# Optimization experiments

Measured on AMD Instinct MI355X. Metric: run time of the kernel, lower is better.

## Reference

```python
import jax, jax.numpy as jnp
import numpy as np

N_HEAD = 16
MASK_VALUE = -10000.0


def setup_inputs() -> dict:
    key = jax.random.key(0)
    k1, k2, k3 = jax.random.split(key, 3)
    B, S, D = 2, 2048, 1024
    x = jax.random.normal(k1, (B, S, D), dtype=jnp.float32)
    W_qkv = jax.random.normal(k2, (D, 3 * D), dtype=jnp.float32) * 0.02
    b_qkv = jnp.zeros((3 * D,), dtype=jnp.float32)
    W_out = jax.random.normal(k3, (D, D), dtype=jnp.float32) * 0.02
    b_out = jnp.zeros((D,), dtype=jnp.float32)
    return {"x": x, "W_qkv": W_qkv, "b_qkv": b_qkv, "W_out": W_out, "b_out": b_out}


def reference(x, W_qkv, b_qkv, W_out, b_out):
    B, S, D = x.shape
    H = N_HEAD
    hd = D // H
    # fused QKV projection
    qkv = x @ W_qkv + b_qkv                      # [B, S, 3D]
    q, k, v = jnp.split(qkv, 3, axis=-1)
    # split heads -> [B, H, S, hd]
    def split_heads(t):
        return t.reshape(B, S, H, hd).transpose(0, 2, 1, 3)
    q, k, v = split_heads(q), split_heads(k), split_heads(v)
    # scaled causal attention with explicit mask-fill (matches ops.attention)
    scale = 1.0 / jnp.sqrt(jnp.asarray(hd, dtype=x.dtype))
    w = jnp.einsum('bhqd,bhkd->bhqk', q, k) * scale   # [B, H, S, S]
    causal = jnp.tril(jnp.ones((S, S), dtype=bool))    # [S, S]
    w = jnp.where(causal, w, jnp.asarray(MASK_VALUE, dtype=w.dtype))
    a = jax.nn.softmax(w, axis=-1)
    o = jnp.einsum('bhqk,bhkd->bhqd', a, v)            # [B, H, S, hd]
    # merge heads -> [B, S, D]
    o = o.transpose(0, 2, 1, 3).reshape(B, S, D)
    out = o @ W_out + b_out
    return out
```

## Files before the change

kernel.cpp:

```cpp
#include <hip/hip_runtime.h>
#include <hip/hip_bf16.h>
#include <stdint.h>

#define BATCH 2
#define SEQ   2048
#define DIM   1024
#define NH    16
#define HD    64
#define MVAL  (-10000.0f)

typedef __attribute__((ext_vector_type(8))) short bf16x8;
typedef __attribute__((ext_vector_type(4))) float f32x4;
typedef unsigned short u16;

static __device__ __forceinline__ u16 f2bf(float f) {
  union { float f; uint32_t u; } c; c.f = f;
  uint32_t x = c.u;
  return (u16)((x + 0x7fffu + ((x >> 16) & 1u)) >> 16);
}

static __device__ __forceinline__ uint32_t pk2(float a, float b) {
  __hip_bfloat162 h = __float22bfloat162_rn(make_float2(a, b));
  union { __hip_bfloat162 h; uint32_t u; } c; c.h = h;
  return c.u;
}

static __device__ __forceinline__ int swz128(int row, int chunk) {
  return row * 128 + (((chunk ^ (row & 7)) & 7) << 4);
}

static __device__ __forceinline__ void gload_lds16(const void* g, void* l) {
  __builtin_amdgcn_global_load_lds((const __attribute__((address_space(1))) void*)g,
                                   (__attribute__((address_space(3))) void*)l, 16, 0, 0);
}

__global__ void cvt_kernel(const float* __restrict__ in, u16* __restrict__ out, int n4) {
  int i = blockIdx.x * blockDim.x + threadIdx.x;
  if (i < n4) {
    float4 v = reinterpret_cast<const float4*>(in)[i];
    reinterpret_cast<uint2*>(out)[i] = make_uint2(pk2(v.x, v.y), pk2(v.z, v.w));
  }
}

__global__ void transpose_cvt_kernel(const float* __restrict__ in, u16* __restrict__ out,
                                     int R, int C) {
  __shared__ float tile[32][33];
  int c0 = blockIdx.x * 32, r0 = blockIdx.y * 32;
  int tx = threadIdx.x, ty = threadIdx.y;
#pragma unroll
  for (int i = 0; i < 32; i += 8)
    tile[ty + i][tx] = in[(size_t)(r0 + ty + i) * C + c0 + tx];
  __syncthreads();
#pragma unroll
  for (int i = 0; i < 32; i += 8)
    out[(size_t)(c0 + ty + i) * R + r0 + tx] = f2bf(tile[tx][ty + i]);
}

template <int EPI>
__global__ __launch_bounds__(256, 2) void gemm_bt_kernel(
    const u16* __restrict__ A, const u16* __restrict__ Bt,
    const float* __restrict__ bias, float* __restrict__ Cout,
    u16* __restrict__ Qo, u16* __restrict__ Ko, u16* __restrict__ Vto,
    int M, int N, int K) {
  __shared__ __align__(16) char lds[32768];
  char* As = lds;
  char* Bs = lds + 16384;
  int tid = threadIdx.x;
  int lane = tid & 63, l15 = lane & 15, l4 = lane >> 4;
  int w = tid >> 6, wr = w >> 1, wc = w & 1;
  int m0 = blockIdx.y * 128, n0 = blockIdx.x * 128;
  int srow = tid >> 3, sch = tid & 7;

  const u16* Ap = A + (size_t)(m0 + srow) * K + sch * 8;
  const u16* Bp = Bt + (size_t)(n0 + srow) * K + sch * 8;

  f32x4 acc[4][4] = {};

  for (int k0 = 0; k0 < K; k0 += 64) {
    __syncthreads();
#pragma unroll
    for (int i = 0; i < 4; i++) {
      gload_lds16(Ap + (size_t)i * 32 * K + k0, As + i * 4096 + tid * 16);
      gload_lds16(Bp + (size_t)i * 32 * K + k0, Bs + i * 4096 + tid * 16);
    }
    __syncthreads();
#pragma unroll
    for (int ks = 0; ks < 2; ks++) {
      int ch = ks * 4 + l4;
      bf16x8 af[4], bfv[4];
#pragma unroll
      for (int mi = 0; mi < 4; mi++)
        af[mi] = *reinterpret_cast<const bf16x8*>(As + (wr * 64 + mi * 16 + l15) * 128 + ch * 16);
#pragma unroll
      for (int nj = 0; nj < 4; nj++)
        bfv[nj] = *reinterpret_cast<const bf16x8*>(Bs + (wc * 64 + nj * 16 + l15) * 128 + ch * 16);
#pragma unroll
      for (int mi = 0; mi < 4; mi++)
#pragma unroll
        for (int nj = 0; nj < 4; nj++)
          acc[mi][nj] = __builtin_amdgcn_mfma_f32_16x16x32_bf16(af[mi], bfv[nj], acc[mi][nj], 0, 0, 0);
    }
  }

#pragma unroll
  for (int nj = 0; nj < 4; nj++) {
    int n = n0 + wc * 64 + nj * 16 + l15;
    float bv = bias[n];
#pragma unroll
    for (int mi = 0; mi < 4; mi++) {
#pragma unroll
      for (int r = 0; r < 4; r++) {
        int m = m0 + wr * 64 + mi * 16 + l4 * 4 + r;
        float v = acc[mi][nj][r] + bv;
        if (EPI == 1) {
          Cout[(size_t)m * N + n] = v;
        } else {
          int b = m >> 11, s = m & 2047;
          int sec = n >> 10, c = n & 1023, h = c >> 6, d = c & 63;
          size_t bh = (size_t)(b * NH + h);
          if (sec == 0)      Qo[(bh * SEQ + s) * HD + d] = f2bf(v * 0.125f);
          else if (sec == 1) Ko[(bh * SEQ + s) * HD + d] = f2bf(v);
          else               Vto[(bh * HD + d) * SEQ + s] = f2bf(v);
        }
      }
    }
  }
}

__global__ __launch_bounds__(256, 2) void attn_kernel(
    const u16* __restrict__ Q, const u16* __restrict__ K,
    const u16* __restrict__ Vt, u16* __restrict__ O) {
  __shared__ __align__(16) char lds[81920];
  int tid = threadIdx.x, lane = tid & 63, w = tid >> 6;
  int l15 = lane & 15, l4 = lane >> 4;
  int sub = w & 1, par = w >> 1;
  int blk = blockIdx.x;
  int bh = (blk & 7) * 4 + ((blk >> 3) & 3);
  int p = blk >> 5;
  const u16* Qh = Q + (size_t)bh * SEQ * HD;
  const u16* Kh = K + (size_t)bh * SEQ * HD;
  const u16* Vh = Vt + (size_t)bh * HD * SEQ;
  char* Pw = lds + 65536 + w * 4096;
  int srow = tid >> 3, sch = tid & 7;
  int b_ = bh >> 4, h_ = bh & 15;

  auto stageKV = [&](int b, int T) {
    const u16* Kt = Kh + (size_t)T * 128 * HD;
    const u16* Vs = Vh + (size_t)T * 128;
    char* Kb = lds + b * 16384;
    char* Vb = lds + 32768 + b * 16384;
#pragma unroll
    for (int i = 0; i < 4; i++) {
      int row = i * 32 + srow;
      int c = (sch ^ (row & 7)) << 3;
      gload_lds16(Kt + (size_t)row * HD + c, Kb + row * 128 + sch * 16);
    }
#pragma unroll
    for (int sv = 0; sv < 2; sv++)
#pragma unroll
      for (int i = 0; i < 2; i++) {
        int d = i * 32 + srow;
        int c = (sch ^ (d & 7)) << 3;
        gload_lds16(Vs + (size_t)d * SEQ + sv * 64 + c, Vb + sv * 8192 + d * 128 + sch * 16);
      }
  };

  int buf = 0;
  stageKV(0, 0);
  __syncthreads();

  for (int pass = 0; pass < 2; pass++) {
    int qt = (pass == 0) ? (31 - p) : p;
    int nT = (qt + 2) >> 1;
    int qb = qt * 64 + sub * 32;

    bf16x8 qf[2][2];
#pragma unroll
    for (int mi = 0; mi < 2; mi++)
#pragma unroll
      for (int ks = 0; ks < 2; ks++)
        qf[mi][ks] = *reinterpret_cast<const bf16x8*>(
            Qh + (size_t)(qb + mi * 16 + l15) * HD + ks * 32 + l4 * 8);

    float mrun[2] = {-1e30f, -1e30f}, lrun[2] = {0.0f, 0.0f};
    f32x4 oacc[4][2] = {};

    for (int T = 0; T < nT; T++) {
      int nxt = (T + 1 < nT) ? (T + 1) : (pass == 0 ? 0 : -1);
      if (nxt >= 0) stageKV(buf ^ 1, nxt);

      char* Kw = lds + buf * 16384 + par * 8192;
      char* Vw = lds + 32768 + buf * 16384 + par * 8192;
      int kvb = T * 128 + par * 64;

      f32x4 s[4][2] = {};
      __builtin_amdgcn_s_setprio(1);
#pragma unroll
      for (int ks = 0; ks < 2; ks++)
#pragma unroll
        for (int nj = 0; nj < 4; nj++) {
          bf16x8 kf = *reinterpret_cast<const bf16x8*>(Kw + swz128(nj * 16 + l15, ks * 4 + l4));
#pragma unroll
          for (int mi = 0; mi < 2; mi++)
            s[nj][mi] = __builtin_amdgcn_mfma_f32_16x16x32_bf16(kf, qf[mi][ks], s[nj][mi], 0, 0, 0);
        }
      __builtin_amdgcn_s_setprio(0);

      if (kvb + 63 > qb) {
#pragma unroll
        for (int nj = 0; nj < 4; nj++)
#pragma unroll
          for (int mi = 0; mi < 2; mi++) {
            int qg = qb + mi * 16 + l15;
#pragma unroll
            for (int r = 0; r < 4; r++) {
              int kg = kvb + nj * 16 + l4 * 4 + r;
              if (kg > qg) s[nj][mi][r] = MVAL;
            }
          }
      }

      float alpha[2];
#pragma unroll
      for (int mi = 0; mi < 2; mi++) {
        float mt = s[0][mi][0];
#pragma unroll
        for (int nj = 0; nj < 4; nj++)
#pragma unroll
          for (int r = 0; r < 4; r++) mt = fmaxf(mt, s[nj][mi][r]);
        mt = fmaxf(mt, __shfl_xor(mt, 16));
        mt = fmaxf(mt, __shfl_xor(mt, 32));
        float mnew = fmaxf(mrun[mi], mt);
        alpha[mi] = __expf(mrun[mi] - mnew);
        mrun[mi] = mnew;
        float rs = 0.0f;
        int prow = mi * 16 + l15;
#pragma unroll
        for (int nj = 0; nj < 4; nj++) {
          float p0 = __expf(s[nj][mi][0] - mnew);
          float p1 = __expf(s[nj][mi][1] - mnew);
          float p2 = __expf(s[nj][mi][2] - mnew);
          float p3 = __expf(s[nj][mi][3] - mnew);
          rs += (p0 + p1) + (p2 + p3);
          int chunk = nj * 2 + (l4 >> 1);
          char* dst = Pw + prow * 128 + (((chunk ^ (prow & 7)) & 7) << 4) + (l4 & 1) * 8;
          *reinterpret_cast<uint2*>(dst) = make_uint2(pk2(p0, p1), pk2(p2, p3));
        }
        rs += __shfl_xor(rs, 16);
        rs += __shfl_xor(rs, 32);
        lrun[mi] = lrun[mi] * alpha[mi] + rs;
      }
#pragma unroll
      for (int nd = 0; nd < 4; nd++)
#pragma unroll
        for (int mi = 0; mi < 2; mi++)
#pragma unroll
          for (int r = 0; r < 4; r++) oacc[nd][mi][r] *= alpha[mi];

      asm volatile("s_waitcnt lgkmcnt(0)" ::: "memory");
      __builtin_amdgcn_sched_barrier(0);

      bf16x8 pf[2][2];
#pragma unroll
      for (int mi = 0; mi < 2; mi++)
#pragma unroll
        for (int ks = 0; ks < 2; ks++)
          pf[mi][ks] = *reinterpret_cast<const bf16x8*>(Pw + swz128(mi * 16 + l15, ks * 4 + l4));

      __builtin_amdgcn_s_setprio(1);
#pragma unroll
      for (int ks = 0; ks < 2; ks++)
#pragma unroll
        for (int nd = 0; nd < 4; nd++) {
          bf16x8 vf = *reinterpret_cast<const bf16x8*>(Vw + swz128(nd * 16 + l15, ks * 4 + l4));
#pragma unroll
          for (int mi = 0; mi < 2; mi++)
            oacc[nd][mi] = __builtin_amdgcn_mfma_f32_16x16x32_bf16(vf, pf[mi][ks], oacc[nd][mi], 0, 0, 0);
        }
      __builtin_amdgcn_s_setprio(0);

      __syncthreads();
      buf ^= 1;
    }

    char* Xo = lds + (buf ^ 1) * 16384;
    float* Xml = (float*)(lds + 65536);
    if (par == 1) {
#pragma unroll
      for (int mi = 0; mi < 2; mi++) {
        int row = sub * 32 + mi * 16 + l15;
        if (l4 == 0) {
          Xml[row * 2] = mrun[mi];
          Xml[row * 2 + 1] = lrun[mi];
        }
#pragma unroll
        for (int nd = 0; nd < 4; nd++)
          *reinterpret_cast<f32x4*>(Xo + row * 256 + (((nd * 4 + l4) ^ (row & 7)) << 4)) =
              oacc[nd][mi];
      }
    }
    __syncthreads();
    if (par == 0) {
#pragma unroll
      for (int mi = 0; mi < 2; mi++) {
        int row = sub * 32 + mi * 16 + l15;
        float mB = Xml[row * 2], lB = Xml[row * 2 + 1];
        float m = fmaxf(mrun[mi], mB);
        float wA = __expf(mrun[mi] - m), wB = __expf(mB - m);
        float linv = 1.0f / (lrun[mi] * wA + lB * wB);
        u16* orow = O + ((size_t)b_ * SEQ + qt * 64 + sub * 32 + mi * 16 + l15) * DIM + h_ * HD;
#pragma unroll
        for (int nd = 0; nd < 4; nd++) {
          f32x4 ob = *reinterpret_cast<const f32x4*>(
              Xo + row * 256 + (((nd * 4 + l4) ^ (row & 7)) << 4));
          float o0 = (oacc[nd][mi][0] * wA + ob[0] * wB) * linv;
          float o1 = (oacc[nd][mi][1] * wA + ob[1] * wB) * linv;
          float o2 = (oacc[nd][mi][2] * wA + ob[2] * wB) * linv;
          float o3 = (oacc[nd][mi][3] * wA + ob[3] * wB) * linv;
          *reinterpret_cast<uint2*>(orow + nd * 16 + l4 * 4) = make_uint2(pk2(o0, o1), pk2(o2, o3));
        }
      }
    }
    __syncthreads();
  }
}

extern "C" void kernel_launch(void* const* d_in, const int* in_sizes, int n_in,
                              void* d_out, int out_size, void* d_ws, size_t ws_size,
                              hipStream_t stream) {
  const float* x     = (const float*)d_in[0];
  const float* W_qkv = (const float*)d_in[1];
  const float* b_qkv = (const float*)d_in[2];
  const float* W_out = (const float*)d_in[3];
  const float* b_out = (const float*)d_in[4];
  float* out = (float*)d_out;
  char* ws = (char*)d_ws;

  u16* xb    = (u16*)(ws);
  u16* WqkvT = (u16*)(ws + 8388608);
  u16* WoutT = (u16*)(ws + 8388608 + 6291456);
  u16* Qb    = (u16*)(ws + 16777216);
  u16* Kb    = (u16*)(ws + 16777216 + 8388608);
  u16* Vtb   = (u16*)(ws + 16777216 + 2 * 8388608);
  u16* Ob    = (u16*)(ws + 16777216 + 3 * 8388608);

  cvt_kernel<<<4096, 256, 0, stream>>>(x, xb, BATCH * SEQ * DIM / 4);
  transpose_cvt_kernel<<<dim3(3 * DIM / 32, DIM / 32), dim3(32, 8), 0, stream>>>(
      W_qkv, WqkvT, DIM, 3 * DIM);
  transpose_cvt_kernel<<<dim3(DIM / 32, DIM / 32), dim3(32, 8), 0, stream>>>(
      W_out, WoutT, DIM, DIM);
  gemm_bt_kernel<0><<<dim3(3 * DIM / 128, BATCH * SEQ / 128), 256, 0, stream>>>(
      xb, WqkvT, b_qkv, nullptr, Qb, Kb, Vtb, BATCH * SEQ, 3 * DIM, DIM);
  attn_kernel<<<512, 256, 0, stream>>>(Qb, Kb, Vtb, Ob);
  gemm_bt_kernel<1><<<dim3(DIM / 128, BATCH * SEQ / 128), 256, 0, stream>>>(
      Ob, WoutT, b_out, out, nullptr, nullptr, nullptr, BATCH * SEQ, DIM, DIM);
}
```

Baseline: 125.5 us.

## Swizzle GEMM LDS, vectorize epilogue stores, move V transpose to separate kernel

```diff
diff --git a/kernel.cpp b/kernel.cpp
--- a/kernel.cpp
+++ b/kernel.cpp
@@ -56,11 +56,36 @@
     out[(size_t)(c0 + ty + i) * R + r0 + tx] = f2bf(tile[tx][ty + i]);
 }
 
+__global__ void vtrans_kernel(const u16* __restrict__ Vi, u16* __restrict__ Vo) {
+  __shared__ __align__(16) char t[8192];
+  int tid = threadIdx.x;
+  int bh = blockIdx.y, s0 = blockIdx.x * 64;
+  const u16* src = Vi + ((size_t)bh * SEQ + s0) * HD;
+#pragma unroll
+  for (int i = 0; i < 2; i++) {
+    int r = i * 32 + (tid >> 3), ch = tid & 7;
+    uint4 v = *reinterpret_cast<const uint4*>(src + (size_t)r * HD + ch * 8);
+    *reinterpret_cast<uint4*>(t + swz128(r, ch)) = v;
+  }
+  __syncthreads();
+  int d = tid >> 2, sc = tid & 3;
+  u16 vals[16];
+#pragma unroll
+  for (int j = 0; j < 16; j++) {
+    int s = sc * 16 + j;
+    vals[j] = *reinterpret_cast<const u16*>(
+        t + s * 128 + ((((d >> 3) ^ (s & 7)) & 7) << 4) + (d & 7) * 2);
+  }
+  u16* dst = Vo + ((size_t)bh * HD + d) * SEQ + s0 + sc * 16;
+  *reinterpret_cast<uint4*>(dst) = *reinterpret_cast<const uint4*>(vals);
+  *reinterpret_cast<uint4*>(dst + 8) = *reinterpret_cast<const uint4*>(vals + 8);
+}
+
 template <int EPI>
 __global__ __launch_bounds__(256, 2) void gemm_bt_kernel(
     const u16* __restrict__ A, const u16* __restrict__ Bt,
     const float* __restrict__ bias, float* __restrict__ Cout,
-    u16* __restrict__ Qo, u16* __restrict__ Ko, u16* __restrict__ Vto,
+    u16* __restrict__ Qo, u16* __restrict__ Ko, u16* __restrict__ Vo,
     int M, int N, int K) {
   __shared__ __align__(16) char lds[32768];
   char* As = lds;
@@ -70,9 +95,10 @@
   int w = tid >> 6, wr = w >> 1, wc = w & 1;
   int m0 = blockIdx.y * 128, n0 = blockIdx.x * 128;
   int srow = tid >> 3, sch = tid & 7;
-
-  const u16* Ap = A + (size_t)(m0 + srow) * K + sch * 8;
-  const u16* Bp = Bt + (size_t)(n0 + srow) * K + sch * 8;
+  int sc_swz = ((sch ^ (srow & 7)) << 3);
+
+  const u16* Ap = A + (size_t)(m0 + srow) * K + sc_swz;
+  const u16* Bp = Bt + (size_t)(n0 + srow) * K + sc_swz;
 
   f32x4 acc[4][4] = {};
 
@@ -90,38 +116,40 @@
       bf16x8 af[4], bfv[4];
 #pragma unroll
       for (int mi = 0; mi < 4; mi++)
-        af[mi] = *reinterpret_cast<const bf16x8*>(As + (wr * 64 + mi * 16 + l15) * 128 + ch * 16);
+        af[mi] = *reinterpret_cast<const bf16x8*>(As + swz128(wr * 64 + mi * 16 + l15, ch));
 #pragma unroll
       for (int nj = 0; nj < 4; nj++)
-        bfv[nj] = *reinterpret_cast<const bf16x8*>(Bs + (wc * 64 + nj * 16 + l15) * 128 + ch * 16);
-#pragma unroll
-      for (int mi = 0; mi < 4; mi++)
-#pragma unroll
-        for (int nj = 0; nj < 4; nj++)
-          acc[mi][nj] = __builtin_amdgcn_mfma_f32_16x16x32_bf16(af[mi], bfv[nj], acc[mi][nj], 0, 0, 0);
+        bfv[nj] = *reinterpret_cast<const bf16x8*>(Bs + swz128(wc * 64 + nj * 16 + l15, ch));
+#pragma unroll
+      for (int nj = 0; nj < 4; nj++)
+#pragma unroll
+        for (int mi = 0; mi < 4; mi++)
+          acc[nj][mi] = __builtin_amdgcn_mfma_f32_16x16x32_bf16(bfv[nj], af[mi], acc[nj][mi], 0, 0, 0);
     }
   }
 
 #pragma unroll
   for (int nj = 0; nj < 4; nj++) {
-    int n = n0 + wc * 64 + nj * 16 + l15;
-    float bv = bias[n];
+    int nb = n0 + wc * 64 + nj * 16 + l4 * 4;
+    float4 bv = *reinterpret_cast<const float4*>(bias + nb);
 #pragma unroll
     for (int mi = 0; mi < 4; mi++) {
-#pragma unroll
-      for (int r = 0; r < 4; r++) {
-        int m = m0 + wr * 64 + mi * 16 + l4 * 4 + r;
-        float v = acc[mi][nj][r] + bv;
-        if (EPI == 1) {
-          Cout[(size_t)m * N + n] = v;
-        } else {
-          int b = m >> 11, s = m & 2047;
-          int sec = n >> 10, c = n & 1023, h = c >> 6, d = c & 63;
-          size_t bh = (size_t)(b * NH + h);
-          if (sec == 0)      Qo[(bh * SEQ + s) * HD + d] = f2bf(v * 0.125f);
-          else if (sec == 1) Ko[(bh * SEQ + s) * HD + d] = f2bf(v);
-          else               Vto[(bh * HD + d) * SEQ + s] = f2bf(v);
-        }
+      int m = m0 + wr * 64 + mi * 16 + l15;
+      f32x4 a = acc[nj][mi];
+      float v0 = a[0] + bv.x, v1 = a[1] + bv.y, v2 = a[2] + bv.z, v3 = a[3] + bv.w;
+      if (EPI == 1) {
+        *reinterpret_cast<float4*>(Cout + (size_t)m * N + nb) = make_float4(v0, v1, v2, v3);
+      } else {
+        int b = m >> 11, s = m & 2047;
+        int sec = nb >> 10, c = nb & 1023, h = c >> 6, d = c & 63;
+        size_t bh = (size_t)(b * NH + h);
+        u16* dst;
+        float scl;
+        if (sec == 0)      { dst = Qo; scl = 0.125f; }
+        else if (sec == 1) { dst = Ko; scl = 1.0f; }
+        else               { dst = Vo; scl = 1.0f; }
+        *reinterpret_cast<uint2*>(dst + (bh * SEQ + s) * HD + d) =
+            make_uint2(pk2(v0 * scl, v1 * scl), pk2(v2 * scl, v3 * scl));
       }
     }
   }
@@ -343,6 +371,7 @@
   u16* Kb    = (u16*)(ws + 16777216 + 8388608);
   u16* Vtb   = (u16*)(ws + 16777216 + 2 * 8388608);
   u16* Ob    = (u16*)(ws + 16777216 + 3 * 8388608);
+  u16* Vraw  = Ob;
 
   cvt_kernel<<<4096, 256, 0, stream>>>(x, xb, BATCH * SEQ * DIM / 4);
   transpose_cvt_kernel<<<dim3(3 * DIM / 32, DIM / 32), dim3(32, 8), 0, stream>>>(
@@ -350,7 +379,8 @@
   transpose_cvt_kernel<<<dim3(DIM / 32, DIM / 32), dim3(32, 8), 0, stream>>>(
       W_out, WoutT, DIM, DIM);
   gemm_bt_kernel<0><<<dim3(3 * DIM / 128, BATCH * SEQ / 128), 256, 0, stream>>>(
-      xb, WqkvT, b_qkv, nullptr, Qb, Kb, Vtb, BATCH * SEQ, 3 * DIM, DIM);
+      xb, WqkvT, b_qkv, nullptr, Qb, Kb, Vraw, BATCH * SEQ, 3 * DIM, DIM);
+  vtrans_kernel<<<dim3(SEQ / 64, BATCH * NH), 256, 0, stream>>>(Vraw, Vtb);
   attn_kernel<<<512, 256, 0, stream>>>(Qb, Kb, Vtb, Ob);
   gemm_bt_kernel<1><<<dim3(DIM / 128, BATCH * SEQ / 128), 256, 0, stream>>>(
       Ob, WoutT, b_out, out, nullptr, nullptr, nullptr, BATCH * SEQ, DIM, DIM);
```

Measured after the change: 127.0 us. No clear change (+1.2%).
